# Optimization experiments

Measured on AMD Instinct MI355X. Metric: run time of the kernel, lower is better.

Reference implementation:

```python
import jax, jax.numpy as jnp
import numpy as np

POLY_DEGREE = 3


def setup_inputs() -> dict:
    key = jax.random.key(0)
    k1, k2, k3 = jax.random.split(key, 3)
    B, L, D = 8192, 16, 4096
    total = sum(L ** d for d in range(POLY_DEGREE + 1))  # 4369
    z = jax.random.normal(k1, (B, L), dtype=jnp.float32)
    W = jax.random.normal(k2, (total, D), dtype=jnp.float32) * 0.02
    b = jax.random.normal(k3, (D,), dtype=jnp.float32) * 0.02
    return {"z": z, "W": W, "b": b}


def poly_features(z):
    # Batched equivalent of per-sample torch.kron chain:
    # degree 0 -> [1]; degree k -> kron(deg_{k-1} feature, z) per sample.
    B = z.shape[0]
    feats = [jnp.ones((B, 1), dtype=z.dtype)]
    cur = z  # degree 1
    feats.append(cur)
    for _ in range(2, POLY_DEGREE + 1):
        # kron(out, latent): (i, j) -> out_i * latent_j
        cur = (cur[:, :, None] * z[:, None, :]).reshape(B, -1)
        feats.append(cur)
    return jnp.concatenate(feats, axis=1)  # [B, total_poly_terms]


def reference(z, W, b):
    x = poly_features(z)          # [B, T]
    return x @ W + b              # [B, data_dim]
```

## Files before the change

kernel.cpp:

```cpp
#include <hip/hip_runtime.h>
#include <hip/hip_bf16.h>

#define NDIM  4096
#define MROWS 8192
#define PREAL 969
#define KP    1024
#define NT    16
#define NWFOLD 1024

typedef unsigned short u16;
typedef __attribute__((ext_vector_type(8))) __bf16 bf16x8;
typedef __attribute__((ext_vector_type(8))) u16 u16x8;
typedef __attribute__((ext_vector_type(4))) float f32x4;

__device__ __forceinline__ u16 bf16rne(float f) {
  unsigned int u = __builtin_bit_cast(unsigned int, f);
  u += 0x7fffu + ((u >> 16) & 1u);
  return (u16)(u >> 16);
}

struct Tbl { int v[KP]; };
constexpr Tbl make_table() {
  Tbl t{};
  for (int p = 0; p < KP; ++p) t.v[p] = -1;
  int p = 0;
  t.v[p++] = (16 << 10) | (16 << 5) | 16;
  for (int i = 0; i < 16; ++i) t.v[p++] = (i << 10) | (16 << 5) | 16;
  for (int i = 0; i < 16; ++i)
    for (int j = i; j < 16; ++j) t.v[p++] = (i << 10) | (j << 5) | 16;
  for (int i = 0; i < 16; ++i)
    for (int j = i; j < 16; ++j)
      for (int k = j; k < 16; ++k) t.v[p++] = (i << 10) | (j << 5) | k;
  return t;
}
__device__ constexpr Tbl TBL = make_table();

__global__ void prep_kernel(const float* __restrict__ z, const float* __restrict__ W,
                            const float* __restrict__ bias,
                            u16* __restrict__ xb, u16* __restrict__ wfbt) {
  __shared__ float tile[64][65];
  __shared__ float zs[17];
  const int bx = blockIdx.x;
  const int tid = threadIdx.x;

  if (bx < NWFOLD) {
    const int p0 = (bx & 15) * 64;
    const int d0 = (bx >> 4) * 64;
    const int d4 = (tid & 15) * 4;
    const int rb = tid >> 4;
    const int dd = d0 + d4;
#pragma unroll
    for (int pp = 0; pp < 4; ++pp) {
      const int r = pp * 16 + rb;
      const int p = p0 + r;
      const int enc = TBL.v[p];
      f32x4 v = {0.f, 0.f, 0.f, 0.f};
      if (enc >= 0) {
        const int i = enc >> 10, j = (enc >> 5) & 31, k = enc & 31;
        if (k == 16) {
          if (j == 16) {
            if (i == 16) {
              v = *reinterpret_cast<const f32x4*>(W + dd);
              f32x4 bb = *reinterpret_cast<const f32x4*>(bias + dd);
              v.x += bb.x; v.y += bb.y; v.z += bb.z; v.w += bb.w;
            } else {
              v = *reinterpret_cast<const f32x4*>(W + (size_t)(1 + i) * NDIM + dd);
            }
          } else {
            v = *reinterpret_cast<const f32x4*>(W + (size_t)(17 + i * 16 + j) * NDIM + dd);
            if (i != j) {
              f32x4 w2 = *reinterpret_cast<const f32x4*>(W + (size_t)(17 + j * 16 + i) * NDIM + dd);
              v.x += w2.x; v.y += w2.y; v.z += w2.z; v.w += w2.w;
            }
          }
        } else {
          int rows[6];
          int nr = 0;
          rows[nr++] = 273 + i * 256 + j * 16 + k;
          if (i == j && j == k) {
          } else if (i == j) {
            rows[nr++] = 273 + i * 256 + k * 16 + i;
            rows[nr++] = 273 + k * 256 + i * 16 + i;
          } else if (j == k) {
            rows[nr++] = 273 + j * 256 + i * 16 + j;
            rows[nr++] = 273 + j * 256 + j * 16 + i;
          } else {
            rows[nr++] = 273 + i * 256 + k * 16 + j;
            rows[nr++] = 273 + j * 256 + i * 16 + k;
            rows[nr++] = 273 + j * 256 + k * 16 + i;
            rows[nr++] = 273 + k * 256 + i * 16 + j;
            rows[nr++] = 273 + k * 256 + j * 16 + i;
          }
          v = *reinterpret_cast<const f32x4*>(W + (size_t)rows[0] * NDIM + dd);
          for (int s = 1; s < nr; ++s) {
            f32x4 w2 = *reinterpret_cast<const f32x4*>(W + (size_t)rows[s] * NDIM + dd);
            v.x += w2.x; v.y += w2.y; v.z += w2.z; v.w += w2.w;
          }
        }
      }
#pragma unroll
      for (int jj = 0; jj < 4; ++jj) tile[r][d4 + jj] = v[jj];
    }
    __syncthreads();
#pragma unroll
    for (int round = 0; round < 2; ++round) {
      const int v = round * 256 + tid;
      const int d = v >> 3;
      const int tg = v & 7;
      u16x8 pack;
#pragma unroll
      for (int e = 0; e < 8; ++e) pack[e] = bf16rne(tile[tg * 8 + e][d]);
      *reinterpret_cast<u16x8*>(wfbt + (size_t)(d0 + d) * KP + p0 + tg * 8) = pack;
    }
  } else {
    const int row = bx - NWFOLD;
    if (tid < 16) zs[tid] = z[row * 16 + tid];
    if (tid == 16) zs[16] = 1.0f;
    __syncthreads();
    u16* xrow = xb + (size_t)row * KP;
    for (int g = tid; g < KP / 8; g += 256) {
      u16x8 pack;
#pragma unroll
      for (int e = 0; e < 8; ++e) {
        const int enc = TBL.v[g * 8 + e];
        float v = 0.0f;
        if (enc >= 0) v = zs[enc >> 10] * (zs[(enc >> 5) & 31] * zs[enc & 31]);
        pack[e] = bf16rne(v);
      }
      *reinterpret_cast<u16x8*>(xrow + g * 8) = pack;
    }
  }
}

#define GLOAD(gp, lp)                                                                     \
  __builtin_amdgcn_global_load_lds((const __attribute__((address_space(1))) unsigned int*)(gp), \
                                   (__attribute__((address_space(3))) unsigned int*)(lp), 16, 0, 0)

__device__ __forceinline__ void bar() {
  asm volatile("" ::: "memory");
  __builtin_amdgcn_s_barrier();
  asm volatile("" ::: "memory");
}

#define VM4 asm volatile("s_waitcnt vmcnt(4)" ::: "memory")
#define VM2 asm volatile("s_waitcnt vmcnt(2)" ::: "memory")
#define VM0 asm volatile("s_waitcnt vmcnt(0)" ::: "memory")

__global__ __launch_bounds__(256, 2) void gemm_kernel(const u16* __restrict__ xb,
                                                      const u16* __restrict__ wbt,
                                                      float* __restrict__ out) {
  __shared__ u16 lds[2 * 16384];

  const int bid  = blockIdx.x;
  const int xcd  = bid & 7;
  const int idx  = bid >> 3;
  const int win  = idx >> 5;
  const int w    = idx & 31;
  const int mtl  = (win >> 2) * 4 + (w >> 3);
  const int ntl  = (win & 3) * 8 + (w & 7);
  const int brow = (xcd * 8 + mtl) * 128;
  const int bcol = ntl * 128;

  const int tid  = threadIdx.x;
  const int lane = tid & 63;
  const int wid  = tid >> 6;
  const int wr   = wid >> 1;
  const int wc   = wid & 1;
  const int f    = lane & 15;
  const int q    = lane >> 4;
  const int f7   = f & 7;

  const int lr = lane >> 3;
  const int swzc = ((lane & 7) ^ lr) * 8;
  const u16* gA = xb  + (size_t)(brow + lr) * KP + swzc;
  const u16* gB = wbt + (size_t)(bcol + lr) * KP + swzc;
  const int qB0 = (wid >> 1) * 64 + (wid & 1) * 16;

#define STGQ(gptr, region, rb, U) do {                                               \
    GLOAD((gptr) + (size_t)(rb) * KP + (U) * 64, (region) + (rb) * 64);              \
    GLOAD((gptr) + (size_t)((rb) + 8) * KP + (U) * 64, (region) + ((rb) + 8) * 64);  \
  } while (0)

#define RD_A(mi, kk) (*reinterpret_cast<const bf16x8*>(bufA + (wr * 64 + (mi) * 16 + f) * 64 + (((kk) * 4 + q) ^ f7) * 8))
#define RD_B(ni, kk) (*reinterpret_cast<const bf16x8*>(bufB + (wc * 64 + (ni) * 16 + f) * 64 + (((kk) * 4 + q) ^ f7) * 8))

#define RDA2(i0) do {                                                                \
    a_[i0][0] = RD_A((i0), 0);     a_[i0][1] = RD_A((i0), 1);                        \
    a_[(i0)+1][0] = RD_A((i0)+1, 0); a_[(i0)+1][1] = RD_A((i0)+1, 1);                \
  } while (0)
#define RDB2(i0) do {                                                                \
    b_[i0][0] = RD_B((i0), 0);     b_[i0][1] = RD_B((i0), 1);                        \
    b_[(i0)+1][0] = RD_B((i0)+1, 0); b_[(i0)+1][1] = RD_B((i0)+1, 1);                \
  } while (0)

#define OCT(M0, N0) do {                                                             \
    __builtin_amdgcn_s_setprio(1);                                                   \
    _Pragma("unroll") for (int _m = 0; _m < 2; ++_m)                                 \
    _Pragma("unroll") for (int _n = 0; _n < 2; ++_n)                                 \
    _Pragma("unroll") for (int _k = 0; _k < 2; ++_k)                                 \
      acc[(M0) + _m][(N0) + _n] = __builtin_amdgcn_mfma_f32_16x16x32_bf16(           \
          a_[(M0) + _m][_k], b_[(N0) + _n][_k], acc[(M0) + _m][(N0) + _n], 0, 0, 0); \
    __builtin_amdgcn_s_setprio(0);                                                   \
  } while (0)

#define TILE_BODY(cA, cB, nA, nB, U) do {                                            \
    bufA = (cA); bufB = (cB);                                                        \
    RDA2(0); RDB2(0); STGQ(gA, (nA), qB0, (U));                                      \
    bar(); OCT(0, 0); VM4; bar();                                                    \
    RDB2(2);          STGQ(gB, (nB), qB0, (U));                                      \
    bar(); OCT(0, 2); VM4; bar();                                                    \
    RDA2(2);          STGQ(gB, (nB), qB0 + 32, (U));                                 \
    bar(); OCT(2, 2); bar();                                                         \
                      STGQ(gA, (nA), qB0 + 32, (U));                                 \
    bar(); OCT(2, 0); VM4; bar();                                                    \
  } while (0)

#define TILE_LAST(cA, cB) do {                                                       \
    bufA = (cA); bufB = (cB);                                                        \
    RDA2(0); RDB2(0);                                                                \
    bar(); OCT(0, 0); VM2; bar();                                                    \
    RDB2(2);                                                                         \
    bar(); OCT(0, 2); VM0; bar();                                                    \
    RDA2(2);                                                                         \
    bar(); OCT(2, 2); bar();                                                         \
    OCT(2, 0);                                                                       \
  } while (0)

  f32x4 acc[4][4] = {};
  bf16x8 a_[4][2], b_[4][2];
  const u16 *bufA, *bufB;

  u16* b0A = lds;            u16* b0B = lds + 8192;
  u16* b1A = lds + 16384;    u16* b1B = b1A + 8192;

  STGQ(gA, b0A, qB0, 0); STGQ(gB, b0B, qB0, 0);
  STGQ(gB, b0B, qB0 + 32, 0); STGQ(gA, b0A, qB0 + 32, 0);
  VM4; bar();

  for (int t = 0; t < NT - 2; t += 2) {
    TILE_BODY(b0A, b0B, b1A, b1B, t + 1);
    TILE_BODY(b1A, b1B, b0A, b0B, t + 2);
  }
  TILE_BODY(b0A, b0B, b1A, b1B, NT - 1);
  TILE_LAST(b1A, b1B);

  const int r0 = brow + wr * 64 + q * 4;
  const int c0 = bcol + wc * 64 + f;
#pragma unroll
  for (int mi = 0; mi < 4; ++mi)
#pragma unroll
    for (int ni = 0; ni < 4; ++ni) {
#pragma unroll
      for (int j = 0; j < 4; ++j)
        out[(size_t)(r0 + mi * 16 + j) * NDIM + (c0 + ni * 16)] = acc[mi][ni][j];
    }
}

__global__ void fallback_kernel(const float* __restrict__ z, const float* __restrict__ W,
                                const float* __restrict__ bias, float* __restrict__ out) {
  __shared__ float feat[4369];
  const int row = blockIdx.x;
  const int tid = threadIdx.x;
  for (int t = tid; t < 4369; t += 256) {
    float v;
    if (t == 0) v = 1.0f;
    else if (t < 17) v = z[row * 16 + t - 1];
    else if (t < 273) { int u = t - 17; v = z[row * 16 + (u >> 4)] * z[row * 16 + (u & 15)]; }
    else { int u = t - 273; v = z[row * 16 + ((u >> 8) & 15)] * (z[row * 16 + ((u >> 4) & 15)] * z[row * 16 + (u & 15)]); }
    feat[t] = v;
  }
  __syncthreads();
  float acc[16];
#pragma unroll
  for (int j = 0; j < 16; ++j) acc[j] = bias[tid + 256 * j];
  for (int t = 0; t < 4369; ++t) {
    const float fv = feat[t];
    const float* wrow = W + (size_t)t * NDIM;
#pragma unroll
    for (int j = 0; j < 16; ++j) acc[j] = fmaf(fv, wrow[tid + 256 * j], acc[j]);
  }
  float* orow = out + (size_t)row * NDIM;
#pragma unroll
  for (int j = 0; j < 16; ++j) orow[tid + 256 * j] = acc[j];
}

extern "C" void kernel_launch(void* const* d_in, const int* in_sizes, int n_in,
                              void* d_out, int out_size, void* d_ws, size_t ws_size,
                              hipStream_t stream) {
  const float* z = (const float*)d_in[0];
  const float* W = (const float*)d_in[1];
  const float* b = (const float*)d_in[2];
  float* out = (float*)d_out;

  const size_t xb_elems  = (size_t)MROWS * KP;
  const size_t wbt_elems = (size_t)NDIM * KP;
  const size_t need = (xb_elems + wbt_elems) * sizeof(u16);

  if (ws_size >= need) {
    u16* xb  = (u16*)d_ws;
    u16* wbt = xb + xb_elems;
    prep_kernel<<<NWFOLD + MROWS, 256, 0, stream>>>(z, W, b, xb, wbt);
    gemm_kernel<<<(MROWS / 128) * (NDIM / 128), 256, 0, stream>>>(xb, wbt, out);
  } else {
    fallback_kernel<<<MROWS, 256, 0, stream>>>(z, W, b, out);
  }
}
```

Before: 104.2 us.

## Switch GEMM mainloop to triple-buffered K=32 tiles with three blocks per CU

Replaces the double-buffered K=64 tile pipeline, with its interleaved quarter-staged loads and many barriers, by a three-stage ring of K=32 tiles. There is one barrier per tile, and loads for the tile two steps ahead are issued before compute. LDS per block shrinks from 64KB to 48KB and launch bounds rise to 3 blocks per CU, aiming for more occupancy and fewer barriers. In exchange each tile does half the MFMA work per sync, with a new XOR swizzle and a different staging layout.

```diff
diff --git a/kernel.cpp b/kernel.cpp
--- a/kernel.cpp
+++ b/kernel.cpp
@@ -5,7 +5,7 @@
 #define MROWS 8192
 #define PREAL 969
 #define KP    1024
-#define NT    16
+#define NT32  32
 #define NWFOLD 1024
 
 typedef unsigned short u16;
@@ -142,14 +142,10 @@
   asm volatile("" ::: "memory");
 }
 
-#define VM4 asm volatile("s_waitcnt vmcnt(4)" ::: "memory")
-#define VM2 asm volatile("s_waitcnt vmcnt(2)" ::: "memory")
-#define VM0 asm volatile("s_waitcnt vmcnt(0)" ::: "memory")
-
-__global__ __launch_bounds__(256, 2) void gemm_kernel(const u16* __restrict__ xb,
+__global__ __launch_bounds__(256, 3) void gemm_kernel(const u16* __restrict__ xb,
                                                       const u16* __restrict__ wbt,
                                                       float* __restrict__ out) {
-  __shared__ u16 lds[2 * 16384];
+  __shared__ u16 lds[3 * 8192];
 
   const int bid  = blockIdx.x;
   const int xcd  = bid & 7;
@@ -168,81 +164,70 @@
   const int wc   = wid & 1;
   const int f    = lane & 15;
   const int q    = lane >> 4;
-  const int f7   = f & 7;
-
-  const int lr = lane >> 3;
-  const int swzc = ((lane & 7) ^ lr) * 8;
-  const u16* gA = xb  + (size_t)(brow + lr) * KP + swzc;
-  const u16* gB = wbt + (size_t)(bcol + lr) * KP + swzc;
-  const int qB0 = (wid >> 1) * 64 + (wid & 1) * 16;
-
-#define STGQ(gptr, region, rb, U) do {                                               \
-    GLOAD((gptr) + (size_t)(rb) * KP + (U) * 64, (region) + (rb) * 64);              \
-    GLOAD((gptr) + (size_t)((rb) + 8) * KP + (U) * 64, (region) + ((rb) + 8) * 64);  \
+  const int fsw  = (f >> 1) & 3;
+
+  const int srow = lane >> 2;
+  const int sch  = ((lane & 3) ^ ((lane >> 3) & 3)) * 8;
+  const u16* gA = xb  + (size_t)(brow + srow) * KP + sch;
+  const u16* gB = wbt + (size_t)(bcol + srow) * KP + sch;
+  const int r1 = wid * 16;
+  const int r2 = 64 + wid * 16;
+
+#define STG_TILE(BUFI, U) do {                                                       \
+    u16* _a = lds + (BUFI) * 8192;                                                   \
+    u16* _b = _a + 4096;                                                             \
+    GLOAD(gA + (size_t)r1 * KP + (U) * 32, _a + r1 * 32);                            \
+    GLOAD(gA + (size_t)r2 * KP + (U) * 32, _a + r2 * 32);                            \
+    GLOAD(gB + (size_t)r1 * KP + (U) * 32, _b + r1 * 32);                            \
+    GLOAD(gB + (size_t)r2 * KP + (U) * 32, _b + r2 * 32);                            \
   } while (0)
 
-#define RD_A(mi, kk) (*reinterpret_cast<const bf16x8*>(bufA + (wr * 64 + (mi) * 16 + f) * 64 + (((kk) * 4 + q) ^ f7) * 8))
-#define RD_B(ni, kk) (*reinterpret_cast<const bf16x8*>(bufB + (wc * 64 + (ni) * 16 + f) * 64 + (((kk) * 4 + q) ^ f7) * 8))
-
-#define RDA2(i0) do {                                                                \
-    a_[i0][0] = RD_A((i0), 0);     a_[i0][1] = RD_A((i0), 1);                        \
-    a_[(i0)+1][0] = RD_A((i0)+1, 0); a_[(i0)+1][1] = RD_A((i0)+1, 1);                \
+#define RD_A(mi) (*reinterpret_cast<const bf16x8*>(bufA + (wr * 64 + (mi) * 16 + f) * 32 + (q ^ fsw) * 8))
+#define RD_B(ni) (*reinterpret_cast<const bf16x8*>(bufB + (wc * 64 + (ni) * 16 + f) * 32 + (q ^ fsw) * 8))
+
+#define TILE_BODY(CUR, STGB, U) do {                                                 \
+    const u16* bufA = lds + (CUR) * 8192;                                            \
+    const u16* bufB = bufA + 4096;                                                   \
+    STG_TILE(STGB, U);                                                               \
+    _Pragma("unroll") for (int _i = 0; _i < 4; ++_i) a_[_i] = RD_A(_i);              \
+    _Pragma("unroll") for (int _i = 0; _i < 4; ++_i) b_[_i] = RD_B(_i);              \
+    __builtin_amdgcn_s_setprio(1);                                                   \
+    _Pragma("unroll") for (int _m = 0; _m < 4; ++_m)                                 \
+    _Pragma("unroll") for (int _n = 0; _n < 4; ++_n)                                 \
+      acc[_m][_n] = __builtin_amdgcn_mfma_f32_16x16x32_bf16(a_[_m], b_[_n], acc[_m][_n], 0, 0, 0); \
+    __builtin_amdgcn_s_setprio(0);                                                   \
+    asm volatile("s_waitcnt vmcnt(4)" ::: "memory");                                 \
+    bar();                                                                           \
   } while (0)
-#define RDB2(i0) do {                                                                \
-    b_[i0][0] = RD_B((i0), 0);     b_[i0][1] = RD_B((i0), 1);                        \
-    b_[(i0)+1][0] = RD_B((i0)+1, 0); b_[(i0)+1][1] = RD_B((i0)+1, 1);                \
+
+#define TILE_NOSTG(CUR, FENCE) do {                                                  \
+    const u16* bufA = lds + (CUR) * 8192;                                            \
+    const u16* bufB = bufA + 4096;                                                   \
+    _Pragma("unroll") for (int _i = 0; _i < 4; ++_i) a_[_i] = RD_A(_i);              \
+    _Pragma("unroll") for (int _i = 0; _i < 4; ++_i) b_[_i] = RD_B(_i);              \
+    __builtin_amdgcn_s_setprio(1);                                                   \
+    _Pragma("unroll") for (int _m = 0; _m < 4; ++_m)                                 \
+    _Pragma("unroll") for (int _n = 0; _n < 4; ++_n)                                 \
+      acc[_m][_n] = __builtin_amdgcn_mfma_f32_16x16x32_bf16(a_[_m], b_[_n], acc[_m][_n], 0, 0, 0); \
+    __builtin_amdgcn_s_setprio(0);                                                   \
+    FENCE;                                                                           \
   } while (0)
 
-#define OCT(M0, N0) do {                                                             \
-    __builtin_amdgcn_s_setprio(1);                                                   \
-    _Pragma("unroll") for (int _m = 0; _m < 2; ++_m)                                 \
-    _Pragma("unroll") for (int _n = 0; _n < 2; ++_n)                                 \
-    _Pragma("unroll") for (int _k = 0; _k < 2; ++_k)                                 \
-      acc[(M0) + _m][(N0) + _n] = __builtin_amdgcn_mfma_f32_16x16x32_bf16(           \
-          a_[(M0) + _m][_k], b_[(N0) + _n][_k], acc[(M0) + _m][(N0) + _n], 0, 0, 0); \
-    __builtin_amdgcn_s_setprio(0);                                                   \
-  } while (0)
-
-#define TILE_BODY(cA, cB, nA, nB, U) do {                                            \
-    bufA = (cA); bufB = (cB);                                                        \
-    RDA2(0); RDB2(0); STGQ(gA, (nA), qB0, (U));                                      \
-    bar(); OCT(0, 0); VM4; bar();                                                    \
-    RDB2(2);          STGQ(gB, (nB), qB0, (U));                                      \
-    bar(); OCT(0, 2); VM4; bar();                                                    \
-    RDA2(2);          STGQ(gB, (nB), qB0 + 32, (U));                                 \
-    bar(); OCT(2, 2); bar();                                                         \
-                      STGQ(gA, (nA), qB0 + 32, (U));                                 \
-    bar(); OCT(2, 0); VM4; bar();                                                    \
-  } while (0)
-
-#define TILE_LAST(cA, cB) do {                                                       \
-    bufA = (cA); bufB = (cB);                                                        \
-    RDA2(0); RDB2(0);                                                                \
-    bar(); OCT(0, 0); VM2; bar();                                                    \
-    RDB2(2);                                                                         \
-    bar(); OCT(0, 2); VM0; bar();                                                    \
-    RDA2(2);                                                                         \
-    bar(); OCT(2, 2); bar();                                                         \
-    OCT(2, 0);                                                                       \
-  } while (0)
-
   f32x4 acc[4][4] = {};
-  bf16x8 a_[4][2], b_[4][2];
-  const u16 *bufA, *bufB;
-
-  u16* b0A = lds;            u16* b0B = lds + 8192;
-  u16* b1A = lds + 16384;    u16* b1B = b1A + 8192;
-
-  STGQ(gA, b0A, qB0, 0); STGQ(gB, b0B, qB0, 0);
-  STGQ(gB, b0B, qB0 + 32, 0); STGQ(gA, b0A, qB0 + 32, 0);
-  VM4; bar();
-
-  for (int t = 0; t < NT - 2; t += 2) {
-    TILE_BODY(b0A, b0B, b1A, b1B, t + 1);
-    TILE_BODY(b1A, b1B, b0A, b0B, t + 2);
-  }
-  TILE_BODY(b0A, b0B, b1A, b1B, NT - 1);
-  TILE_LAST(b1A, b1B);
+  bf16x8 a_[4], b_[4];
+
+  STG_TILE(0, 0);
+  STG_TILE(1, 1);
+  asm volatile("s_waitcnt vmcnt(4)" ::: "memory");
+  bar();
+
+  for (int t3 = 0; t3 < 30; t3 += 3) {
+    TILE_BODY(0, 2, t3 + 2);
+    TILE_BODY(1, 0, t3 + 3);
+    TILE_BODY(2, 1, t3 + 4);
+  }
+  TILE_NOSTG(0, { asm volatile("s_waitcnt vmcnt(0)" ::: "memory"); bar(); });
+  TILE_NOSTG(1, {});
 
   const int r0 = brow + wr * 64 + q * 4;
   const int c0 = bcol + wc * 64 + f;
```

Result: slower. 112.0 us (+7.5%).

## Load A fragments directly to registers and triple-buffer B in LDS

Applied to the files above, without the earlier changes.

A-operand tiles are no longer staged through LDS. Each wave now loads its MFMA A fragments straight from global memory into double-buffered registers one tile ahead. The freed LDS is used to triple-buffer the B tiles, which cuts LDS use per block. That allows a launch bound of 3 blocks per CU, and each tile has one barrier instead of several split phases. In exchange the A loads are uncoalesced, A rows are re-fetched by both column waves, and register pressure rises, which may limit occupancy.

```diff
diff --git a/kernel.cpp b/kernel.cpp
--- a/kernel.cpp
+++ b/kernel.cpp
@@ -143,13 +143,12 @@
 }
 
 #define VM4 asm volatile("s_waitcnt vmcnt(4)" ::: "memory")
-#define VM2 asm volatile("s_waitcnt vmcnt(2)" ::: "memory")
 #define VM0 asm volatile("s_waitcnt vmcnt(0)" ::: "memory")
 
-__global__ __launch_bounds__(256, 2) void gemm_kernel(const u16* __restrict__ xb,
+__global__ __launch_bounds__(256, 3) void gemm_kernel(const u16* __restrict__ xb,
                                                       const u16* __restrict__ wbt,
                                                       float* __restrict__ out) {
-  __shared__ u16 lds[2 * 16384];
+  __shared__ u16 lds[3 * 8192];
 
   const int bid  = blockIdx.x;
   const int xcd  = bid & 7;
@@ -172,77 +171,76 @@
 
   const int lr = lane >> 3;
   const int swzc = ((lane & 7) ^ lr) * 8;
-  const u16* gA = xb  + (size_t)(brow + lr) * KP + swzc;
   const u16* gB = wbt + (size_t)(bcol + lr) * KP + swzc;
-  const int qB0 = (wid >> 1) * 64 + (wid & 1) * 16;
-
-#define STGQ(gptr, region, rb, U) do {                                               \
-    GLOAD((gptr) + (size_t)(rb) * KP + (U) * 64, (region) + (rb) * 64);              \
-    GLOAD((gptr) + (size_t)((rb) + 8) * KP + (U) * 64, (region) + ((rb) + 8) * 64);  \
+  const int sb = wid * 32;
+
+#define STG_B(BUFI, U) do {                                                          \
+    u16* _b = lds + (BUFI) * 8192;                                                   \
+    GLOAD(gB + (size_t)(sb +  0) * KP + (U) * 64, _b + (sb +  0) * 64);              \
+    GLOAD(gB + (size_t)(sb +  8) * KP + (U) * 64, _b + (sb +  8) * 64);              \
+    GLOAD(gB + (size_t)(sb + 16) * KP + (U) * 64, _b + (sb + 16) * 64);              \
+    GLOAD(gB + (size_t)(sb + 24) * KP + (U) * 64, _b + (sb + 24) * 64);              \
   } while (0)
 
-#define RD_A(mi, kk) (*reinterpret_cast<const bf16x8*>(bufA + (wr * 64 + (mi) * 16 + f) * 64 + (((kk) * 4 + q) ^ f7) * 8))
+  const u16* gAf = xb + (size_t)(brow + wr * 64 + f) * KP + q * 8;
+
+#define LDA_FRAGS(DST, U) do {                                                       \
+    _Pragma("unroll") for (int _m = 0; _m < 4; ++_m)                                 \
+    _Pragma("unroll") for (int _k = 0; _k < 2; ++_k)                                 \
+      DST[_m][_k] = *reinterpret_cast<const bf16x8*>(                                \
+          gAf + (size_t)(_m * 16) * KP + (U) * 64 + _k * 32);                        \
+  } while (0)
+
 #define RD_B(ni, kk) (*reinterpret_cast<const bf16x8*>(bufB + (wc * 64 + (ni) * 16 + f) * 64 + (((kk) * 4 + q) ^ f7) * 8))
 
-#define RDA2(i0) do {                                                                \
-    a_[i0][0] = RD_A((i0), 0);     a_[i0][1] = RD_A((i0), 1);                        \
-    a_[(i0)+1][0] = RD_A((i0)+1, 0); a_[(i0)+1][1] = RD_A((i0)+1, 1);                \
-  } while (0)
-#define RDB2(i0) do {                                                                \
-    b_[i0][0] = RD_B((i0), 0);     b_[i0][1] = RD_B((i0), 1);                        \
-    b_[(i0)+1][0] = RD_B((i0)+1, 0); b_[(i0)+1][1] = RD_B((i0)+1, 1);                \
-  } while (0)
-
-#define OCT(M0, N0) do {                                                             \
+#define MFMA_TILE(ACUR) do {                                                         \
+    _Pragma("unroll") for (int _i = 0; _i < 4; ++_i) {                               \
+      b_[_i][0] = RD_B(_i, 0); b_[_i][1] = RD_B(_i, 1); }                            \
     __builtin_amdgcn_s_setprio(1);                                                   \
-    _Pragma("unroll") for (int _m = 0; _m < 2; ++_m)                                 \
-    _Pragma("unroll") for (int _n = 0; _n < 2; ++_n)                                 \
+    _Pragma("unroll") for (int _m = 0; _m < 4; ++_m)                                 \
+    _Pragma("unroll") for (int _n = 0; _n < 4; ++_n)                                 \
     _Pragma("unroll") for (int _k = 0; _k < 2; ++_k)                                 \
-      acc[(M0) + _m][(N0) + _n] = __builtin_amdgcn_mfma_f32_16x16x32_bf16(           \
-          a_[(M0) + _m][_k], b_[(N0) + _n][_k], acc[(M0) + _m][(N0) + _n], 0, 0, 0); \
+      acc[_m][_n] = __builtin_amdgcn_mfma_f32_16x16x32_bf16(                         \
+          ACUR[_m][_k], b_[_n][_k], acc[_m][_n], 0, 0, 0);                           \
     __builtin_amdgcn_s_setprio(0);                                                   \
   } while (0)
 
-#define TILE_BODY(cA, cB, nA, nB, U) do {                                            \
-    bufA = (cA); bufB = (cB);                                                        \
-    RDA2(0); RDB2(0); STGQ(gA, (nA), qB0, (U));                                      \
-    bar(); OCT(0, 0); VM4; bar();                                                    \
-    RDB2(2);          STGQ(gB, (nB), qB0, (U));                                      \
-    bar(); OCT(0, 2); VM4; bar();                                                    \
-    RDA2(2);          STGQ(gB, (nB), qB0 + 32, (U));                                 \
-    bar(); OCT(2, 2); bar();                                                         \
-                      STGQ(gA, (nA), qB0 + 32, (U));                                 \
-    bar(); OCT(2, 0); VM4; bar();                                                    \
+#define TILE_STD(CUR, STGB, U2, ACUR, ANXT) do {                                     \
+    const u16* bufB = lds + (CUR) * 8192;                                            \
+    LDA_FRAGS(ANXT, (U2) - 1);                                                       \
+    STG_B(STGB, U2);                                                                 \
+    MFMA_TILE(ACUR);                                                                 \
+    VM4; bar();                                                                      \
   } while (0)
 
-#define TILE_LAST(cA, cB) do {                                                       \
-    bufA = (cA); bufB = (cB);                                                        \
-    RDA2(0); RDB2(0);                                                                \
-    bar(); OCT(0, 0); VM2; bar();                                                    \
-    RDB2(2);                                                                         \
-    bar(); OCT(0, 2); VM0; bar();                                                    \
-    RDA2(2);                                                                         \
-    bar(); OCT(2, 2); bar();                                                         \
-    OCT(2, 0);                                                                       \
-  } while (0)
-
   f32x4 acc[4][4] = {};
-  bf16x8 a_[4][2], b_[4][2];
-  const u16 *bufA, *bufB;
-
-  u16* b0A = lds;            u16* b0B = lds + 8192;
-  u16* b1A = lds + 16384;    u16* b1B = b1A + 8192;
-
-  STGQ(gA, b0A, qB0, 0); STGQ(gB, b0B, qB0, 0);
-  STGQ(gB, b0B, qB0 + 32, 0); STGQ(gA, b0A, qB0 + 32, 0);
+  bf16x8 aEv[4][2], aOd[4][2], b_[4][2];
+
+  STG_B(0, 0);
+  LDA_FRAGS(aEv, 0);
+  STG_B(1, 1);
   VM4; bar();
 
-  for (int t = 0; t < NT - 2; t += 2) {
-    TILE_BODY(b0A, b0B, b1A, b1B, t + 1);
-    TILE_BODY(b1A, b1B, b0A, b0B, t + 2);
-  }
-  TILE_BODY(b0A, b0B, b1A, b1B, NT - 1);
-  TILE_LAST(b1A, b1B);
+  for (int t6 = 0; t6 < 12; t6 += 6) {
+    TILE_STD(0, 2, t6 + 2, aEv, aOd);
+    TILE_STD(1, 0, t6 + 3, aOd, aEv);
+    TILE_STD(2, 1, t6 + 4, aEv, aOd);
+    TILE_STD(0, 2, t6 + 5, aOd, aEv);
+    TILE_STD(1, 0, t6 + 6, aEv, aOd);
+    TILE_STD(2, 1, t6 + 7, aOd, aEv);
+  }
+  TILE_STD(0, 2, 14, aEv, aOd);
+  TILE_STD(1, 0, 15, aOd, aEv);
+  {
+    const u16* bufB = lds + 2 * 8192;
+    LDA_FRAGS(aOd, 15);
+    MFMA_TILE(aEv);
+    VM0; bar();
+  }
+  {
+    const u16* bufB = lds;
+    MFMA_TILE(aOd);
+  }
 
   const int r0 = brow + wr * 64 + q * 4;
   const int c0 = bcol + wc * 64 + f;
```

New measurement: 243.1 us. 2.33x slower.
